# Performance work log

Hardware: AMD Instinct MI355X
Metric: run time of the kernel (lower is better)

## Reference

```python
import jax, jax.numpy as jnp
import numpy as np

N_NODES = 50000
N_EDGES = 1280000
N_GRAPHS = 64
IN_CH = 6
HID = 64
SLOPE = 0.2  # LeakyReLU negative slope


def _lrelu(x):
    return jax.nn.leaky_relu(x, SLOPE)


def _edge_conv(x, src, dst, W1, b1, W2, b2):
    # PyG EdgeConv: message = nn([x_i, x_j - x_i]); x_i = x[dst], x_j = x[src]; max-aggr onto dst
    xi = x[dst]                                   # [E, F]
    m = jnp.concatenate([xi, x[src] - xi], -1)    # [E, 2F]
    h = _lrelu(_lrelu(m @ W1 + b1) @ W2 + b2)     # [E, H]
    agg = jax.ops.segment_max(h, dst, num_segments=N_NODES)
    return jnp.where(jnp.isneginf(agg), 0.0, agg)  # nodes with no in-edges -> 0


def setup_inputs() -> dict:
    key = jax.random.key(0)
    ks = jax.random.split(key, 12)
    glorot = lambda k, fi, fo: jax.random.normal(k, (fi, fo), jnp.float32) * np.sqrt(2.0 / (fi + fo))
    x = jax.random.normal(ks[0], (N_NODES, IN_CH), jnp.float32)
    edge_index = jax.random.randint(ks[1], (2, N_EDGES), 0, N_NODES, jnp.int64 if jax.config.x64_enabled else jnp.int32)
    batch = jnp.sort(jax.random.randint(ks[2], (N_NODES,), 0, N_GRAPHS))
    return {
        "x": x, "edge_index": edge_index, "batch": batch,
        "W1": glorot(ks[3], 2 * IN_CH, HID), "b1": jnp.zeros((HID,), jnp.float32),
        "W2": glorot(ks[4], HID, HID),       "b2": jnp.zeros((HID,), jnp.float32),
        "W3": glorot(ks[5], 2 * HID, HID),   "b3": jnp.zeros((HID,), jnp.float32),
        "W4": glorot(ks[6], HID, HID),       "b4": jnp.zeros((HID,), jnp.float32),
        "Wc1": glorot(ks[7], 2 * HID, HID),  "bc1": jnp.zeros((HID,), jnp.float32),
        "Wc2": glorot(ks[8], HID, 1),        "bc2": jnp.zeros((1,), jnp.float32),
    }


def reference(x, edge_index, batch, W1, b1, W2, b2, W3, b3, W4, b4, Wc1, bc1, Wc2, bc2):
    src, dst = edge_index[0], edge_index[1]
    h = _edge_conv(x, src, dst, W1, b1, W2, b2)   # [N, H]
    h = _edge_conv(h, src, dst, W3, b3, W4, b4)   # [N, H]
    # global mean + max pool per graph
    cnt = jax.ops.segment_sum(jnp.ones((N_NODES,), h.dtype), batch, num_segments=N_GRAPHS)
    mean_p = jax.ops.segment_sum(h, batch, num_segments=N_GRAPHS) / jnp.clip(cnt, 1.0)[:, None]
    max_p = jax.ops.segment_max(h, batch, num_segments=N_GRAPHS)
    max_p = jnp.where(jnp.isneginf(max_p), 0.0, max_p)
    g = jnp.concatenate([mean_p, max_p], -1)      # [G, 2H]
    logits = _lrelu(g @ Wc1 + bc1) @ Wc2 + bc2    # dropout is identity at inference
    return logits.squeeze(-1)                      # [G]
```

## Files before the change

### kernel.cpp

```cpp
#include <hip/hip_runtime.h>
#include <hip/hip_bf16.h>

#define SLOPE 0.2f
#define NPB 64
#define CAP 2048
#define SUBCAP 384
#define MAXBUCK 1024
#define EPB 4096
#define XF1B 512
#define PPARTS 16

typedef _Float16 f16x8  __attribute__((ext_vector_type(8)));
typedef float    f32x4  __attribute__((ext_vector_type(4)));
typedef unsigned u32;
typedef unsigned u32x4  __attribute__((ext_vector_type(4)));

__device__ __forceinline__ float lrelu(float v) { return fmaxf(v, SLOPE * v); }

__device__ __forceinline__ float lane_bcast(float v, int k) {
    return __int_as_float(__builtin_amdgcn_readlane(__float_as_int(v), k));
}

__device__ __forceinline__ f16x8 lrelu8(f16x8 v) {
    f16x8 s = v * (_Float16)SLOPE;
#if __has_builtin(__builtin_elementwise_max)
    return __builtin_elementwise_max(v, s);
#else
    f16x8 r;
#pragma unroll
    for (int i = 0; i < 8; ++i) r[i] = v[i] > s[i] ? v[i] : s[i];
    return r;
#endif
}

__device__ __forceinline__ void split_f16(float v, _Float16& h, _Float16& l) {
    h = (_Float16)v;
    l = (_Float16)(v - (float)h);
}
__device__ __forceinline__ u32 pack_f16(_Float16 a, _Float16 b) {
    return (u32)__builtin_bit_cast(unsigned short, a) |
           ((u32)__builtin_bit_cast(unsigned short, b) << 16);
}

__global__ void __launch_bounds__(256) scatter_xform1_kernel(
    const int* __restrict__ srcI, const int* __restrict__ dstI,
    int* __restrict__ cursor, u32* __restrict__ pairW,
    int E, int nNodes, int nBuck, int nCntB,
    const float* __restrict__ x,
    const float* __restrict__ W1, const float* __restrict__ b1,
    _Float16* __restrict__ Ph, _Float16* __restrict__ Qh)
{
    if (blockIdx.x < nCntB) {
        __shared__ int cnt4[4][MAXBUCK];
        __shared__ int base[MAXBUCK];
// ... 68 lines not shown
        }
        return;
    }
    const int lane = threadIdx.x & 63;
    const int wave = ((blockIdx.x - nCntB) * 256 + threadIdx.x) >> 6;
    const int nw   = (XF1B * 256) >> 6;

    float wd[6], wb[6];
#pragma unroll
    for (int r = 0; r < 6; ++r) {
        wb[r] = W1[(6 + r) * 64 + lane];
        wd[r] = W1[r * 64 + lane] - wb[r];
    }
    const float bb = b1[lane];
    for (int i = wave; i < nNodes; i += nw) {
        const float* xr = x + (size_t)i * 6;
        float p = bb, q = 0.f;
#pragma unroll
        for (int r = 0; r < 6; ++r) {
            float xv = xr[r];
            p = fmaf(xv, wd[r], p);
            q = fmaf(xv, wb[r], q);
        }
        Ph[(size_t)i * 64 + lane] = (_Float16)p;
        Qh[(size_t)i * 64 + lane] = (_Float16)q;
    }
}

__global__ void __launch_bounds__(256) bucket_sort_kernel(
    const u32* __restrict__ pairW, const int* __restrict__ cursor,
    int2* __restrict__ rowInfo, int* __restrict__ sortedSrc, int nNodes)
{
    __shared__ u32 pairLds[CAP];
    __shared__ int nodeCnt[NPB];
    __shared__ int nodeCur[NPB];
    __shared__ int wcS[8];
    __shared__ int wBase[9];
    const int b   = blockIdx.x;
    const int n0  = b * NPB;
    const int n1  = min(n0 + NPB, nNodes);
    const int tid = threadIdx.x;

    if (tid < NPB) nodeCnt[tid] = 0;
    if (tid < 8) wcS[tid] = min(cursor[b * 8 + tid], SUBCAP);
    __syncthreads();
    if (tid == 0) {
        int acc = 0;
#pragma unroll
        for (int jj = 0; jj < 8; ++jj) { wBase[jj] = acc; acc += wcS[jj]; }
        wBase[8] = acc;
    }
    __syncthreads();

#pragma unroll
    for (int jj = 0; jj < 8; ++jj) {
        const int w0 = (b * 8 + jj) * SUBCAP;
        const int wc = wcS[jj];
        const int d0 = wBase[jj];
        const int nv = wc >> 2;
        const u32x4* p4 = (const u32x4*)(pairW + w0);
        for (int i = tid; i < nv; i += 256) {
            const u32x4 v = p4[i];
            pairLds[d0 + i * 4 + 0] = v[0];
            pairLds[d0 + i * 4 + 1] = v[1];
            pairLds[d0 + i * 4 + 2] = v[2];
            pairLds[d0 + i * 4 + 3] = v[3];
        }
        for (int i = (nv << 2) + tid; i < wc; i += 256)
            pairLds[d0 + i] = pairW[w0 + i];
    }
    __syncthreads();

    const int total = wBase[8];
    for (int i = tid; i < total; i += 256)
        atomicAdd(&nodeCnt[pairLds[i] & (NPB - 1)], 1);
    __syncthreads();
    if (tid < 64) {
        const int c = nodeCnt[tid];
        int inc = c;
#pragma unroll
        for (int off = 1; off < 64; off <<= 1) {
            int t = __shfl_up(inc, off);
            if (tid >= off) inc += t;
        }
        const int st = b * CAP + inc - c;
        nodeCur[tid] = st;
        if (tid < n1 - n0) rowInfo[n0 + tid] = make_int2(st, c);
    }
    __syncthreads();
    for (int i = tid; i < total; i += 256) {
        const u32 w = pairLds[i];
        const int pos = atomicAdd(&nodeCur[w & (NPB - 1)], 1);
        sortedSrc[pos] = (int)(w >> 6);
    }
}

__global__ void __launch_bounds__(256) node_xform2_kernel(
    const _Float16* __restrict__ B1h,
    const float* __restrict__ W3, const float* __restrict__ b3,
    _Float16* __restrict__ Ph, _Float16* __restrict__ Qh, int nNodes)
{
    const int lane = threadIdx.x & 63;
    const int wave = (blockIdx.x * blockDim.x + threadIdx.x) >> 6;
    const int nw   = (gridDim.x * blockDim.x) >> 6;

    float wd[64], wb[64];
#pragma unroll
    for (int k = 0; k < 64; ++k) {
        wb[k] = W3[(64 + k) * 64 + lane];
        wd[k] = W3[k * 64 + lane] - wb[k];
    }
    const float bb = b3[lane];

    for (int i = wave; i < nNodes; i += nw) {
        const float a = (float)B1h[(size_t)i * 64 + lane];
        float p0 = bb, p1 = 0.f, p2 = 0.f, p3 = 0.f;
        float q0 = 0.f, q1 = 0.f, q2 = 0.f, q3 = 0.f;
#pragma unroll
        for (int k = 0; k < 64; k += 4) {
            float a0 = lane_bcast(a, k);
            float a1 = lane_bcast(a, k + 1);
            float a2 = lane_bcast(a, k + 2);
            float a3 = lane_bcast(a, k + 3);
            p0 = fmaf(a0, wd[k],     p0);  q0 = fmaf(a0, wb[k],     q0);
            p1 = fmaf(a1, wd[k + 1], p1);  q1 = fmaf(a1, wb[k + 1], q1);
            p2 = fmaf(a2, wd[k + 2], p2);  q2 = fmaf(a2, wb[k + 2], q2);
            p3 = fmaf(a3, wd[k + 3], p3);  q3 = fmaf(a3, wb[k + 3], q3);
        }
        Ph[(size_t)i * 64 + lane] = (_Float16)((p0 + p1) + (p2 + p3));
        Qh[(size_t)i * 64 + lane] = (_Float16)((q0 + q1) + (q2 + q3));
    }
}

__global__ void __launch_bounds__(256) edge_agg_mfma_kernel(
    const _Float16* __restrict__ Ph, const _Float16* __restrict__ Qh,
    const int2* __restrict__ rowInfo, const int* __restrict__ sortedSrc,
    const float* __restrict__ W, const float* __restrict__ b,
    _Float16* __restrict__ outB, int nNodes)
{
    __shared__ u32x4 wlds[16][64];

    const int tid  = threadIdx.x;
    const int lane = tid & 63;
    const int cn   = lane & 15;
    const int q    = lane >> 4;
    const int wv   = tid >> 6;
    const int wave = (blockIdx.x * 256 + tid) >> 6;
    const int nw   = (gridDim.x * 256) >> 6;

#pragma unroll
    for (int i = 0; i < 4; ++i) {
        const int f    = wv + i * 4;
        const int isLo = f >> 3;
        const int g    = f & 7;
        const int nt   = g >> 1;
        const int ks   = g & 1;
        u32x4 d;
#pragma unroll
        for (int p = 0; p < 4; ++p) {
            float w0 = W[(ks * 32 + q * 8 + 2 * p)     * 64 + nt * 16 + cn];
            float w1 = W[(ks * 32 + q * 8 + 2 * p + 1) * 64 + nt * 16 + cn];
            _Float16 h0, l0, h1, l1;
            split_f16(w0, h0, l0);
            split_f16(w1, h1, l1);
            d[p] = isLo ? pack_f16(l0, l1) : pack_f16(h0, h1);
        }
        wlds[f][lane] = d;
    }
    float bc[4];
#pragma unroll
    for (int nt = 0; nt < 4; ++nt) bc[nt] = b[nt * 16 + cn];
    __syncthreads();

    const u32 nClamp = (u32)(nNodes - 1);
    const int nPairs = (nNodes + 1) >> 1;

    for (int t = wave; t < nPairs; t += nw) {
        const int n1 = 2 * t;
        const int n2 = 2 * t + 1;
        const bool has2 = (n2 < nNodes);

        const int2 ri1 = rowInfo[n1];
        const int2 ri2 = has2 ? rowInfo[n2] : make_int2(ri1.x, 0);
        const int rs1  = __builtin_amdgcn_readfirstlane(ri1.x);
        const int deg1 = __builtin_amdgcn_readfirstlane(ri1.y);
        const int rs2  = __builtin_amdgcn_readfirstlane(ri2.x);
        const int deg2 = __builtin_amdgcn_readfirstlane(ri2.y);
        const int d1c = max(deg1, 1) - 1;
        const int d2c = max(deg2, 1) - 1;

        const f16x8* P1 = (const f16x8*)(Ph + (size_t)n1 * 64);
        const f16x8* P2 = (const f16x8*)(Ph + (size_t)(has2 ? n2 : n1) * 64);
        const f16x8 p1A = P1[q], p1B = P1[4 + q];
        const f16x8 p2A = P2[q], p2B = P2[4 + q];

        float m10 = -INFINITY, m11 = -INFINITY, m12 = -INFINITY, m13 = -INFINITY;
        float m20 = -INFINITY, m21 = -INFINITY, m22 = -INFINITY, m23 = -INFINITY;

        const int gmax = max(deg1, deg2);
        for (int g0 = 0; g0 < gmax; g0 += 32) {
            u32 sA1 = (u32)sortedSrc[rs1 + min(g0 + cn,      d1c)];
            u32 sB1 = (u32)sortedSrc[rs1 + min(g0 + 16 + cn, d1c)];
            u32 sA2 = (u32)sortedSrc[rs2 + min(g0 + cn,      d2c)];
            u32 sB2 = (u32)sortedSrc[rs2 + min(g0 + 16 + cn, d2c)];
            sA1 = min(sA1, nClamp); sB1 = min(sB1, nClamp);
            sA2 = min(sA2, nClamp); sB2 = min(sB2, nClamp);
            const f16x8* QA1 = (const f16x8*)(Qh + (size_t)sA1 * 64);
            const f16x8* QB1 = (const f16x8*)(Qh + (size_t)sB1 * 64);
            const f16x8* QA2 = (const f16x8*)(Qh + (size_t)sA2 * 64);
            const f16x8* QB2 = (const f16x8*)(Qh + (size_t)sB2 * 64);
            const f16x8 qA1a = QA1[q], qA1b = QA1[4 + q];
            const f16x8 qB1a = QB1[q], qB1b = QB1[4 + q];
            const f16x8 qA2a = QA2[q], qA2b = QA2[4 + q];
            const f16x8 qB2a = QB2[q], qB2b = QB2[4 + q];

            if (g0 < deg1) {
                const f16x8 A00 = lrelu8(p1A + qA1a);
                const f16x8 A01 = lrelu8(p1B + qA1b);
                const f16x8 A10 = lrelu8(p1A + qB1a);
                const f16x8 A11 = lrelu8(p1B + qB1b);
#pragma unroll
                for (int nt = 0; nt < 4; ++nt) {
                    const f16x8 wh0 = __builtin_bit_cast(f16x8, wlds[nt * 2][lane]);
                    const f16x8 wh1 = __builtin_bit_cast(f16x8, wlds[nt * 2 + 1][lane]);
                    const f16x8 wl0 = __builtin_bit_cast(f16x8, wlds[8 + nt * 2][lane]);
                    const f16x8 wl1 = __builtin_bit_cast(f16x8, wlds[8 + nt * 2 + 1][lane]);
                    f32x4 a; a[0] = a[1] = a[2] = a[3] = bc[nt];
                    a = __builtin_amdgcn_mfma_f32_16x16x32_f16(A00, wl0, a, 0, 0, 0);
                    a = __builtin_amdgcn_mfma_f32_16x16x32_f16(A00, wh0, a, 0, 0, 0);
                    a = __builtin_amdgcn_mfma_f32_16x16x32_f16(A01, wl1, a, 0, 0, 0);
                    a = __builtin_amdgcn_mfma_f32_16x16x32_f16(A01, wh1, a, 0, 0, 0);
                    f32x4 c; c[0] = c[1] = c[2] = c[3] = bc[nt];
                    c = __builtin_amdgcn_mfma_f32_16x16x32_f16(A10, wl0, c, 0, 0, 0);
                    c = __builtin_amdgcn_mfma_f32_16x16x32_f16(A10, wh0, c, 0, 0, 0);
                    c = __builtin_amdgcn_mfma_f32_16x16x32_f16(A11, wl1, c, 0, 0, 0);
                    c = __builtin_amdgcn_mfma_f32_16x16x32_f16(A11, wh1, c, 0, 0, 0);
                    float m = (nt == 0) ? m10 : (nt == 1) ? m11 : (nt == 2) ? m12 : m13;
                    m = fmaxf(m, fmaxf(fmaxf(a[0], a[1]), fmaxf(a[2], a[3])));
                    m = fmaxf(m, fmaxf(fmaxf(c[0], c[1]), fmaxf(c[2], c[3])));
                    if (nt == 0) m10 = m; else if (nt == 1) m11 = m;
                    else if (nt == 2) m12 = m; else m13 = m;
                }
            }
            if (g0 < deg2) {
                const f16x8 A00 = lrelu8(p2A + qA2a);
                const f16x8 A01 = lrelu8(p2B + qA2b);
                const f16x8 A10 = lrelu8(p2A + qB2a);
                const f16x8 A11 = lrelu8(p2B + qB2b);
#pragma unroll
                for (int nt = 0; nt < 4; ++nt) {
                    const f16x8 wh0 = __builtin_bit_cast(f16x8, wlds[nt * 2][lane]);
                    const f16x8 wh1 = __builtin_bit_cast(f16x8, wlds[nt * 2 + 1][lane]);
                    const f16x8 wl0 = __builtin_bit_cast(f16x8, wlds[8 + nt * 2][lane]);
                    const f16x8 wl1 = __builtin_bit_cast(f16x8, wlds[8 + nt * 2 + 1][lane]);
                    f32x4 a; a[0] = a[1] = a[2] = a[3] = bc[nt];
                    a = __builtin_amdgcn_mfma_f32_16x16x32_f16(A00, wl0, a, 0, 0, 0);
                    a = __builtin_amdgcn_mfma_f32_16x16x32_f16(A00, wh0, a, 0, 0, 0);
                    a = __builtin_amdgcn_mfma_f32_16x16x32_f16(A01, wl1, a, 0, 0, 0);
                    a = __builtin_amdgcn_mfma_f32_16x16x32_f16(A01, wh1, a, 0, 0, 0);
                    f32x4 c; c[0] = c[1] = c[2] = c[3] = bc[nt];
                    c = __builtin_amdgcn_mfma_f32_16x16x32_f16(A10, wl0, c, 0, 0, 0);
                    c = __builtin_amdgcn_mfma_f32_16x16x32_f16(A10, wh0, c, 0, 0, 0);
                    c = __builtin_amdgcn_mfma_f32_16x16x32_f16(A11, wl1, c, 0, 0, 0);
                    c = __builtin_amdgcn_mfma_f32_16x16x32_f16(A11, wh1, c, 0, 0, 0);
                    float m = (nt == 0) ? m20 : (nt == 1) ? m21 : (nt == 2) ? m22 : m23;
                    m = fmaxf(m, fmaxf(fmaxf(a[0], a[1]), fmaxf(a[2], a[3])));
                    m = fmaxf(m, fmaxf(fmaxf(c[0], c[1]), fmaxf(c[2], c[3])));
                    if (nt == 0) m20 = m; else if (nt == 1) m21 = m;
                    else if (nt == 2) m22 = m; else m23 = m;
                }
            }
        }

        m10 = fmaxf(m10, __shfl_xor(m10, 16)); m10 = fmaxf(m10, __shfl_xor(m10, 32));
        m11 = fmaxf(m11, __shfl_xor(m11, 16)); m11 = fmaxf(m11, __shfl_xor(m11, 32));
        m12 = fmaxf(m12, __shfl_xor(m12, 16)); m12 = fmaxf(m12, __shfl_xor(m12, 32));
        m13 = fmaxf(m13, __shfl_xor(m13, 16)); m13 = fmaxf(m13, __shfl_xor(m13, 32));
        float sel1 = (q < 2) ? ((q == 0) ? m10 : m11) : ((q == 2) ? m12 : m13);
        outB[(size_t)n1 * 64 + q * 16 + cn] =
            (_Float16)((deg1 > 0) ? lrelu(sel1) : 0.0f);

        if (has2) {
            m20 = fmaxf(m20, __shfl_xor(m20, 16)); m20 = fmaxf(m20, __shfl_xor(m20, 32));
            m21 = fmaxf(m21, __shfl_xor(m21, 16)); m21 = fmaxf(m21, __shfl_xor(m21, 32));
            m22 = fmaxf(m22, __shfl_xor(m22, 16)); m22 = fmaxf(m22, __shfl_xor(m22, 32));
            m23 = fmaxf(m23, __shfl_xor(m23, 16)); m23 = fmaxf(m23, __shfl_xor(m23, 32));
            float sel2 = (q < 2) ? ((q == 0) ? m20 : m21) : ((q == 2) ? m22 : m23);
            outB[(size_t)n2 * 64 + q * 16 + cn] =
                (_Float16)((deg2 > 0) ? lrelu(sel2) : 0.0f);
        }
    }
}

__device__ __forceinline__ int lower_bound_i(const int* __restrict__ a, int n, int key)
{
    int lo = 0, hi = n;
    while (lo < hi) {
        int mid = (lo + hi) >> 1;
        if (a[mid] < key) lo = mid + 1; else hi = mid;
    }
    return lo;
}

__global__ void __launch_bounds__(256) pool_kernel(
    const _Float16* __restrict__ Bh, const int* __restrict__ batch,
    float* __restrict__ gpart, int nNodes)
{
    const int gid  = blockIdx.x / PPARTS;
    const int part = blockIdx.x % PPARTS;
    const int c    = threadIdx.x & 63;
    const int wid  = threadIdx.x >> 6;

    const int s = lower_bound_i(batch, nNodes, gid);
    const int e = lower_bound_i(batch, nNodes, gid + 1);
    const int len = e - s;
    const int ps = s + (len * part) / PPARTS;
    const int pe = s + (len * (part + 1)) / PPARTS;

    float sum = 0.f, mx = -INFINITY;
    for (int n = ps + wid; n < pe; n += 4) {
        float v = (float)Bh[(size_t)n * 64 + c];
        sum += v;
        mx = fmaxf(mx, v);
// ... 68 lines not shown
    const float* bc2 = (const float*)d_in[14];
    float* out = (float*)d_out;

    const int nNodes  = in_sizes[0] / 6;
    const int E       = in_sizes[1] / 2;
    const int nGraphs = out_size;
    const int* srcI = ei;
    const int* dstI = ei + E;
    const int nBuck = (nNodes + NPB - 1) / NPB;
    const int nCntB = (E + EPB - 1) / EPB;

    char* wsp = (char*)d_ws;
    size_t off = 0;
    int*  cursor    = (int*)(wsp + off);   off = align_up(off + (size_t)MAXBUCK * 8 * 4, 256);
    int2* rowInfo   = (int2*)(wsp + off);  off = align_up(off + (size_t)nNodes * 8, 256);
    int*  sortedSrc = (int*)(wsp + off);   off = align_up(off + (size_t)nBuck * CAP * 4, 256);
    u32*  pairW     = (u32*)(wsp + off);   off = align_up(off + (size_t)nBuck * 8 * SUBCAP * 4, 256);
    const size_t nFeat = (size_t)nNodes * 64;
    _Float16* Ph   = (_Float16*)(wsp + off);  off = align_up(off + nFeat * 2, 256);
    _Float16* Qh   = (_Float16*)(wsp + off);  off = align_up(off + nFeat * 2, 256);
    _Float16* B1h  = (_Float16*)(wsp + off);  off = align_up(off + nFeat * 2, 256);
    _Float16* B2h  = (_Float16*)(wsp + off);  off = align_up(off + nFeat * 2, 256);
    float*    gpart= (float*)(wsp + off);     off = align_up(off + (size_t)nGraphs * PPARTS * 132 * 4, 256);
    (void)ws_size;

    (void)hipMemsetAsync(cursor, 0, (size_t)nBuck * 8 * 4, stream);
    scatter_xform1_kernel<<<nCntB + XF1B, 256, 0, stream>>>(
        srcI, dstI, cursor, pairW, E, nNodes, nBuck, nCntB, x, W1, b1, Ph, Qh);
    bucket_sort_kernel<<<nBuck, 256, 0, stream>>>(pairW, cursor, rowInfo,
                                                  sortedSrc, nNodes);

    edge_agg_mfma_kernel<<<2048, 256, 0, stream>>>(Ph, Qh, rowInfo, sortedSrc,
                                                   W2, b2, B1h, nNodes);
    node_xform2_kernel<<<2048, 256, 0, stream>>>(B1h, W3, b3, Ph, Qh, nNodes);
    edge_agg_mfma_kernel<<<2048, 256, 0, stream>>>(Ph, Qh, rowInfo, sortedSrc,
                                                   W4, b4, B2h, nNodes);

    pool_kernel<<<nGraphs * PPARTS, 256, 0, stream>>>(B2h, batch, gpart, nNodes);
    cls_kernel<<<nGraphs, 64, 0, stream>>>(gpart, Wc1, bc1, Wc2, bc2, out);
}
```

Baseline: 267.7 us.

## Software-pipeline edge aggregation with one node per wave and prefetched gathers

The edge aggregation kernel now gives each wave one destination node per iteration instead of a pair, and software-pipelines across iterations. It prefetches the next node's row info, source indices, P row and first batch of Q gathers while computing the current node. This aims to hide gather latency without the wasted lanes and divergence that come from processing two nodes of unequal degree together. It also adds an occupancy hint to the launch bounds, which may limit registers and cause spills given the larger set of live prefetch buffers.

```diff
diff --git a/kernel.cpp b/kernel.cpp
--- a/kernel.cpp
+++ b/kernel.cpp
@@ -254,7 +254,7 @@
     }
 }
 
-__global__ void __launch_bounds__(256) edge_agg_mfma_kernel(
+__global__ void __launch_bounds__(256, 4) edge_agg_mfma_kernel(
     const _Float16* __restrict__ Ph, const _Float16* __restrict__ Qh,
     const int2* __restrict__ rowInfo, const int* __restrict__ sortedSrc,
     const float* __restrict__ W, const float* __restrict__ b,
@@ -294,122 +294,121 @@
     for (int nt = 0; nt < 4; ++nt) bc[nt] = b[nt * 16 + cn];
     __syncthreads();
 
+    if (wave >= nNodes) return;
+
     const u32 nClamp = (u32)(nNodes - 1);
-    const int nPairs = (nNodes + 1) >> 1;
-
-    for (int t = wave; t < nPairs; t += nw) {
-        const int n1 = 2 * t;
-        const int n2 = 2 * t + 1;
-        const bool has2 = (n2 < nNodes);
-
-        const int2 ri1 = rowInfo[n1];
-        const int2 ri2 = has2 ? rowInfo[n2] : make_int2(ri1.x, 0);
-        const int rs1  = __builtin_amdgcn_readfirstlane(ri1.x);
-        const int deg1 = __builtin_amdgcn_readfirstlane(ri1.y);
-        const int rs2  = __builtin_amdgcn_readfirstlane(ri2.x);
-        const int deg2 = __builtin_amdgcn_readfirstlane(ri2.y);
-        const int d1c = max(deg1, 1) - 1;
-        const int d2c = max(deg2, 1) - 1;
-
-        const f16x8* P1 = (const f16x8*)(Ph + (size_t)n1 * 64);
-        const f16x8* P2 = (const f16x8*)(Ph + (size_t)(has2 ? n2 : n1) * 64);
-        const f16x8 p1A = P1[q], p1B = P1[4 + q];
-        const f16x8 p2A = P2[q], p2B = P2[4 + q];
-
-        float m10 = -INFINITY, m11 = -INFINITY, m12 = -INFINITY, m13 = -INFINITY;
-        float m20 = -INFINITY, m21 = -INFINITY, m22 = -INFINITY, m23 = -INFINITY;
-
-        const int gmax = max(deg1, deg2);
-        for (int g0 = 0; g0 < gmax; g0 += 32) {
-            u32 sA1 = (u32)sortedSrc[rs1 + min(g0 + cn,      d1c)];
-            u32 sB1 = (u32)sortedSrc[rs1 + min(g0 + 16 + cn, d1c)];
-            u32 sA2 = (u32)sortedSrc[rs2 + min(g0 + cn,      d2c)];
-            u32 sB2 = (u32)sortedSrc[rs2 + min(g0 + 16 + cn, d2c)];
-            sA1 = min(sA1, nClamp); sB1 = min(sB1, nClamp);
-            sA2 = min(sA2, nClamp); sB2 = min(sB2, nClamp);
-            const f16x8* QA1 = (const f16x8*)(Qh + (size_t)sA1 * 64);
-            const f16x8* QB1 = (const f16x8*)(Qh + (size_t)sB1 * 64);
-            const f16x8* QA2 = (const f16x8*)(Qh + (size_t)sA2 * 64);
-            const f16x8* QB2 = (const f16x8*)(Qh + (size_t)sB2 * 64);
-            const f16x8 qA1a = QA1[q], qA1b = QA1[4 + q];
-            const f16x8 qB1a = QB1[q], qB1b = QB1[4 + q];
-            const f16x8 qA2a = QA2[q], qA2b = QA2[4 + q];
-            const f16x8 qB2a = QB2[q], qB2b = QB2[4 + q];
-
-            if (g0 < deg1) {
-                const f16x8 A00 = lrelu8(p1A + qA1a);
-                const f16x8 A01 = lrelu8(p1B + qA1b);
-                const f16x8 A10 = lrelu8(p1A + qB1a);
-                const f16x8 A11 = lrelu8(p1B + qB1b);
-#pragma unroll
-                for (int nt = 0; nt < 4; ++nt) {
-                    const f16x8 wh0 = __builtin_bit_cast(f16x8, wlds[nt * 2][lane]);
-                    const f16x8 wh1 = __builtin_bit_cast(f16x8, wlds[nt * 2 + 1][lane]);
-                    const f16x8 wl0 = __builtin_bit_cast(f16x8, wlds[8 + nt * 2][lane]);
-                    const f16x8 wl1 = __builtin_bit_cast(f16x8, wlds[8 + nt * 2 + 1][lane]);
-                    f32x4 a; a[0] = a[1] = a[2] = a[3] = bc[nt];
-                    a = __builtin_amdgcn_mfma_f32_16x16x32_f16(A00, wl0, a, 0, 0, 0);
-                    a = __builtin_amdgcn_mfma_f32_16x16x32_f16(A00, wh0, a, 0, 0, 0);
-                    a = __builtin_amdgcn_mfma_f32_16x16x32_f16(A01, wl1, a, 0, 0, 0);
-                    a = __builtin_amdgcn_mfma_f32_16x16x32_f16(A01, wh1, a, 0, 0, 0);
-                    f32x4 c; c[0] = c[1] = c[2] = c[3] = bc[nt];
-                    c = __builtin_amdgcn_mfma_f32_16x16x32_f16(A10, wl0, c, 0, 0, 0);
-                    c = __builtin_amdgcn_mfma_f32_16x16x32_f16(A10, wh0, c, 0, 0, 0);
-                    c = __builtin_amdgcn_mfma_f32_16x16x32_f16(A11, wl1, c, 0, 0, 0);
-                    c = __builtin_amdgcn_mfma_f32_16x16x32_f16(A11, wh1, c, 0, 0, 0);
-                    float m = (nt == 0) ? m10 : (nt == 1) ? m11 : (nt == 2) ? m12 : m13;
-                    m = fmaxf(m, fmaxf(fmaxf(a[0], a[1]), fmaxf(a[2], a[3])));
-                    m = fmaxf(m, fmaxf(fmaxf(c[0], c[1]), fmaxf(c[2], c[3])));
-                    if (nt == 0) m10 = m; else if (nt == 1) m11 = m;
-                    else if (nt == 2) m12 = m; else m13 = m;
-                }
+    const int nLast  = nNodes - 1;
+
+    auto loadIdx = [&](int rs, int dc, int g0, u32& sA, u32& sB) {
+        sA = (u32)sortedSrc[rs + min(g0 + cn, dc)];
+        sB = (u32)sortedSrc[rs + min(g0 + 16 + cn, dc)];
+    };
+    auto loadQ = [&](u32 sA, u32 sB, f16x8& qAa, f16x8& qAb,
+                     f16x8& qBa, f16x8& qBb) {
+        const f16x8* QA = (const f16x8*)(Qh + (size_t)min(sA, nClamp) * 64);
+        const f16x8* QB = (const f16x8*)(Qh + (size_t)min(sB, nClamp) * 64);
+        qAa = QA[q]; qAb = QA[4 + q];
+        qBa = QB[q]; qBb = QB[4 + q];
+    };
+    auto loadP = [&](int t, f16x8& pA, f16x8& pB) {
+        const f16x8* P = (const f16x8*)(Ph + (size_t)t * 64);
+        pA = P[q]; pB = P[4 + q];
+    };
+    auto compute32 = [&](f16x8 pA, f16x8 pB,
+                         f16x8 qAa, f16x8 qAb, f16x8 qBa, f16x8 qBb,
+                         float& m0, float& m1, float& m2, float& m3) {
+        const f16x8 A00 = lrelu8(pA + qAa);
+        const f16x8 A01 = lrelu8(pB + qAb);
+        const f16x8 A10 = lrelu8(pA + qBa);
+        const f16x8 A11 = lrelu8(pB + qBb);
+#pragma unroll
+        for (int nt = 0; nt < 4; ++nt) {
+            const f16x8 wh0 = __builtin_bit_cast(f16x8, wlds[nt * 2][lane]);
+            const f16x8 wh1 = __builtin_bit_cast(f16x8, wlds[nt * 2 + 1][lane]);
+            const f16x8 wl0 = __builtin_bit_cast(f16x8, wlds[8 + nt * 2][lane]);
+            const f16x8 wl1 = __builtin_bit_cast(f16x8, wlds[8 + nt * 2 + 1][lane]);
+            f32x4 a; a[0] = a[1] = a[2] = a[3] = bc[nt];
+            a = __builtin_amdgcn_mfma_f32_16x16x32_f16(A00, wl0, a, 0, 0, 0);
+            a = __builtin_amdgcn_mfma_f32_16x16x32_f16(A00, wh0, a, 0, 0, 0);
+            a = __builtin_amdgcn_mfma_f32_16x16x32_f16(A01, wl1, a, 0, 0, 0);
+            a = __builtin_amdgcn_mfma_f32_16x16x32_f16(A01, wh1, a, 0, 0, 0);
+            f32x4 c; c[0] = c[1] = c[2] = c[3] = bc[nt];
+            c = __builtin_amdgcn_mfma_f32_16x16x32_f16(A10, wl0, c, 0, 0, 0);
+            c = __builtin_amdgcn_mfma_f32_16x16x32_f16(A10, wh0, c, 0, 0, 0);
+            c = __builtin_amdgcn_mfma_f32_16x16x32_f16(A11, wl1, c, 0, 0, 0);
+            c = __builtin_amdgcn_mfma_f32_16x16x32_f16(A11, wh1, c, 0, 0, 0);
+            float m = (nt == 0) ? m0 : (nt == 1) ? m1 : (nt == 2) ? m2 : m3;
+            m = fmaxf(fmaxf(fmaxf(a[0], a[1]), a[2]), fmaxf(a[3], m));
+            m = fmaxf(fmaxf(fmaxf(c[0], c[1]), c[2]), fmaxf(c[3], m));
+            if (nt == 0) m0 = m; else if (nt == 1) m1 = m;
+            else if (nt == 2) m2 = m; else m3 = m;
+        }
+    };
+
+    f16x8 q0Aa, q0Ab, q0Ba, q0Bb, p0A, p0B;  u32 s0A, s0B;
+    f16x8 q1Aa, q1Ab, q1Ba, q1Bb, p1A, p1B;  u32 s1A, s1B;
+    int2 riN;
+    int rs0, dg0, rs1, dg1;
+
+    {
+        const int2 riA = rowInfo[wave];
+        const int2 riB = rowInfo[min(wave + nw, nLast)];
+        rs0 = __builtin_amdgcn_readfirstlane(riA.x);
+        dg0 = __builtin_amdgcn_readfirstlane(riA.y);
+        rs1 = __builtin_amdgcn_readfirstlane(riB.x);
+        dg1 = __builtin_amdgcn_readfirstlane(riB.y);
+        loadIdx(rs0, max(dg0, 1) - 1, 0, s0A, s0B);
+        loadP(wave, p0A, p0B);
+        loadQ(s0A, s0B, q0Aa, q0Ab, q0Ba, q0Bb);
+        loadIdx(rs1, max(dg1, 1) - 1, 0, s1A, s1B);
+        loadP(min(wave + nw, nLast), p1A, p1B);
+        riN = rowInfo[min(wave + 2 * nw, nLast)];
+    }
+
+    auto iter = [&](int tc, int rsC, int dgC, int& rs2, int& dg2,
+                    f16x8& qCAa, f16x8& qCAb, f16x8& qCBa, f16x8& qCBb,
+                    f16x8& pCA, f16x8& pCB, u32& sCA, u32& sCB,
+                    f16x8& qNAa, f16x8& qNAb, f16x8& qNBa, f16x8& qNBb,
+                    u32 sNA, u32 sNB) {
+        loadQ(sNA, sNB, qNAa, qNAb, qNBa, qNBb);
+        rs2 = __builtin_amdgcn_readfirstlane(riN.x);
+        dg2 = __builtin_amdgcn_readfirstlane(riN.y);
+        loadIdx(rs2, max(dg2, 1) - 1, 0, sCA, sCB);
+        riN = rowInfo[min(tc + 3 * nw, nLast)];
+        float m0 = -INFINITY, m1 = -INFINITY, m2 = -INFINITY, m3 = -INFINITY;
+        if (dgC > 0) {
+            compute32(pCA, pCB, qCAa, qCAb, qCBa, qCBb, m0, m1, m2, m3);
+            const int dcC = dgC - 1;
+            for (int g0 = 32; g0 < dgC; g0 += 32) {
+                u32 eA, eB;
+                loadIdx(rsC, dcC, g0, eA, eB);
+                f16x8 eAa, eAb, eBa, eBb;
+                loadQ(eA, eB, eAa, eAb, eBa, eBb);
+                compute32(pCA, pCB, eAa, eAb, eBa, eBb, m0, m1, m2, m3);
             }
-            if (g0 < deg2) {
-                const f16x8 A00 = lrelu8(p2A + qA2a);
-                const f16x8 A01 = lrelu8(p2B + qA2b);
-                const f16x8 A10 = lrelu8(p2A + qB2a);
-                const f16x8 A11 = lrelu8(p2B + qB2b);
-#pragma unroll
-                for (int nt = 0; nt < 4; ++nt) {
-                    const f16x8 wh0 = __builtin_bit_cast(f16x8, wlds[nt * 2][lane]);
-                    const f16x8 wh1 = __builtin_bit_cast(f16x8, wlds[nt * 2 + 1][lane]);
-                    const f16x8 wl0 = __builtin_bit_cast(f16x8, wlds[8 + nt * 2][lane]);
-                    const f16x8 wl1 = __builtin_bit_cast(f16x8, wlds[8 + nt * 2 + 1][lane]);
-                    f32x4 a; a[0] = a[1] = a[2] = a[3] = bc[nt];
-                    a = __builtin_amdgcn_mfma_f32_16x16x32_f16(A00, wl0, a, 0, 0, 0);
-                    a = __builtin_amdgcn_mfma_f32_16x16x32_f16(A00, wh0, a, 0, 0, 0);
-                    a = __builtin_amdgcn_mfma_f32_16x16x32_f16(A01, wl1, a, 0, 0, 0);
-                    a = __builtin_amdgcn_mfma_f32_16x16x32_f16(A01, wh1, a, 0, 0, 0);
-                    f32x4 c; c[0] = c[1] = c[2] = c[3] = bc[nt];
-                    c = __builtin_amdgcn_mfma_f32_16x16x32_f16(A10, wl0, c, 0, 0, 0);
-                    c = __builtin_amdgcn_mfma_f32_16x16x32_f16(A10, wh0, c, 0, 0, 0);
-                    c = __builtin_amdgcn_mfma_f32_16x16x32_f16(A11, wl1, c, 0, 0, 0);
-                    c = __builtin_amdgcn_mfma_f32_16x16x32_f16(A11, wh1, c, 0, 0, 0);
-                    float m = (nt == 0) ? m20 : (nt == 1) ? m21 : (nt == 2) ? m22 : m23;
-                    m = fmaxf(m, fmaxf(fmaxf(a[0], a[1]), fmaxf(a[2], a[3])));
-                    m = fmaxf(m, fmaxf(fmaxf(c[0], c[1]), fmaxf(c[2], c[3])));
-                    if (nt == 0) m20 = m; else if (nt == 1) m21 = m;
-                    else if (nt == 2) m22 = m; else m23 = m;
-                }
-            }
-        }
-
-        m10 = fmaxf(m10, __shfl_xor(m10, 16)); m10 = fmaxf(m10, __shfl_xor(m10, 32));
-        m11 = fmaxf(m11, __shfl_xor(m11, 16)); m11 = fmaxf(m11, __shfl_xor(m11, 32));
-        m12 = fmaxf(m12, __shfl_xor(m12, 16)); m12 = fmaxf(m12, __shfl_xor(m12, 32));
-        m13 = fmaxf(m13, __shfl_xor(m13, 16)); m13 = fmaxf(m13, __shfl_xor(m13, 32));
-        float sel1 = (q < 2) ? ((q == 0) ? m10 : m11) : ((q == 2) ? m12 : m13);
-        outB[(size_t)n1 * 64 + q * 16 + cn] =
-            (_Float16)((deg1 > 0) ? lrelu(sel1) : 0.0f);
-
-        if (has2) {
-            m20 = fmaxf(m20, __shfl_xor(m20, 16)); m20 = fmaxf(m20, __shfl_xor(m20, 32));
-            m21 = fmaxf(m21, __shfl_xor(m21, 16)); m21 = fmaxf(m21, __shfl_xor(m21, 32));
-            m22 = fmaxf(m22, __shfl_xor(m22, 16)); m22 = fmaxf(m22, __shfl_xor(m22, 32));
-            m23 = fmaxf(m23, __shfl_xor(m23, 16)); m23 = fmaxf(m23, __shfl_xor(m23, 32));
-            float sel2 = (q < 2) ? ((q == 0) ? m20 : m21) : ((q == 2) ? m22 : m23);
-            outB[(size_t)n2 * 64 + q * 16 + cn] =
-                (_Float16)((deg2 > 0) ? lrelu(sel2) : 0.0f);
+        }
+        loadP(min(tc + 2 * nw, nLast), pCA, pCB);
+        m0 = fmaxf(m0, __shfl_xor(m0, 16)); m0 = fmaxf(m0, __shfl_xor(m0, 32));
+        m1 = fmaxf(m1, __shfl_xor(m1, 16)); m1 = fmaxf(m1, __shfl_xor(m1, 32));
+        m2 = fmaxf(m2, __shfl_xor(m2, 16)); m2 = fmaxf(m2, __shfl_xor(m2, 32));
+        m3 = fmaxf(m3, __shfl_xor(m3, 16)); m3 = fmaxf(m3, __shfl_xor(m3, 32));
+        const float sel = (q < 2) ? ((q == 0) ? m0 : m1)
+                                  : ((q == 2) ? m2 : m3);
+        outB[(size_t)tc * 64 + q * 16 + cn] =
+            (_Float16)((dgC > 0) ? lrelu(sel) : 0.0f);
+    };
+
+    for (int t = wave; t < nNodes; t += 2 * nw) {
+        int rs2, dg2;
+        iter(t, rs0, dg0, rs2, dg2,
+             q0Aa, q0Ab, q0Ba, q0Bb, p0A, p0B, s0A, s0B,
+             q1Aa, q1Ab, q1Ba, q1Bb, s1A, s1B);
+        rs0 = rs2; dg0 = dg2;
+        if (t + nw < nNodes) {
+            iter(t + nw, rs1, dg1, rs2, dg2,
+                 q1Aa, q1Ab, q1Ba, q1Bb, p1A, p1B, s1A, s1B,
+                 q0Aa, q0Ab, q0Ba, q0Bb, s0A, s0B);
+            rs1 = rs2; dg1 = dg2;
         }
     }
 }
```

Measured after the change: 468.6 us. 1.75x slower.

## Software-pipeline row info and source index loads across node-pair iterations

Applied to the files above, without the earlier changes.

Restructures the edge aggregation loop so that the rowInfo for the pair two iterations ahead and the first 32 sortedSrc indices for the next pair are loaded ahead of time and carried in registers. The first 32-edge chunk is then processed straight from the prefetched indices, and later chunks fall back to the original per-chunk loads. This targets the dependent load chain (rowInfo, then sortedSrc, then Qh) that stalls each wave at the start of every pair, at the cost of more live registers and extra prefetch loads. The MFMA body is factored into a macro, with a small reordering of the max reduction.

```diff
diff --git a/kernel.cpp b/kernel.cpp
--- a/kernel.cpp
+++ b/kernel.cpp
@@ -254,6 +254,37 @@
     }
 }
 
+
+#define COMPUTE32(PA, PB, QA0, QA1, QB0, QB1, M0, M1, M2, M3)                  \
+  {                                                                            \
+    const f16x8 A00_ = lrelu8((PA) + (QA0));                                   \
+    const f16x8 A01_ = lrelu8((PB) + (QA1));                                   \
+    const f16x8 A10_ = lrelu8((PA) + (QB0));                                   \
+    const f16x8 A11_ = lrelu8((PB) + (QB1));                                   \
+    _Pragma("unroll")                                                          \
+    for (int nt_ = 0; nt_ < 4; ++nt_) {                                        \
+      const f16x8 wh0_ = __builtin_bit_cast(f16x8, wlds[nt_ * 2][lane]);       \
+      const f16x8 wh1_ = __builtin_bit_cast(f16x8, wlds[nt_ * 2 + 1][lane]);   \
+      const f16x8 wl0_ = __builtin_bit_cast(f16x8, wlds[8 + nt_ * 2][lane]);   \
+      const f16x8 wl1_ = __builtin_bit_cast(f16x8, wlds[8 + nt_ * 2 + 1][lane]); \
+      f32x4 a_; a_[0] = a_[1] = a_[2] = a_[3] = bc[nt_];                       \
+      a_ = __builtin_amdgcn_mfma_f32_16x16x32_f16(A00_, wl0_, a_, 0, 0, 0);    \
+      a_ = __builtin_amdgcn_mfma_f32_16x16x32_f16(A00_, wh0_, a_, 0, 0, 0);    \
+      a_ = __builtin_amdgcn_mfma_f32_16x16x32_f16(A01_, wl1_, a_, 0, 0, 0);    \
+      a_ = __builtin_amdgcn_mfma_f32_16x16x32_f16(A01_, wh1_, a_, 0, 0, 0);    \
+      f32x4 c_; c_[0] = c_[1] = c_[2] = c_[3] = bc[nt_];                       \
+      c_ = __builtin_amdgcn_mfma_f32_16x16x32_f16(A10_, wl0_, c_, 0, 0, 0);    \
+      c_ = __builtin_amdgcn_mfma_f32_16x16x32_f16(A10_, wh0_, c_, 0, 0, 0);    \
+      c_ = __builtin_amdgcn_mfma_f32_16x16x32_f16(A11_, wl1_, c_, 0, 0, 0);    \
+      c_ = __builtin_amdgcn_mfma_f32_16x16x32_f16(A11_, wh1_, c_, 0, 0, 0);    \
+      float m_ = (nt_ == 0) ? (M0) : (nt_ == 1) ? (M1) : (nt_ == 2) ? (M2) : (M3); \
+      m_ = fmaxf(fmaxf(fmaxf(a_[0], a_[1]), a_[2]), fmaxf(a_[3], m_));         \
+      m_ = fmaxf(fmaxf(fmaxf(c_[0], c_[1]), c_[2]), fmaxf(c_[3], m_));         \
+      if (nt_ == 0) (M0) = m_; else if (nt_ == 1) (M1) = m_;                   \
+      else if (nt_ == 2) (M2) = m_; else (M3) = m_;                            \
+    }                                                                          \
+  }
+
 __global__ void __launch_bounds__(256) edge_agg_mfma_kernel(
     const _Float16* __restrict__ Ph, const _Float16* __restrict__ Qh,
     const int2* __restrict__ rowInfo, const int* __restrict__ sortedSrc,
@@ -294,104 +325,93 @@
     for (int nt = 0; nt < 4; ++nt) bc[nt] = b[nt * 16 + cn];
     __syncthreads();
 
+    const int nPairs = (nNodes + 1) >> 1;
+    if (wave >= nPairs) return;
     const u32 nClamp = (u32)(nNodes - 1);
-    const int nPairs = (nNodes + 1) >> 1;
+    const int nLastN = nNodes - 1;
+    const int pLast  = nPairs - 1;
+
+    int rs1, dg1, rs2, dg2;
+    u32 sA1, sB1, sA2, sB2;
+    int2 riNa, riNb;
+
+    {
+        const int n1 = 2 * wave;
+        const int2 r1 = rowInfo[n1];
+        const int2 r2 = rowInfo[min(n1 + 1, nLastN)];
+        rs1 = __builtin_amdgcn_readfirstlane(r1.x);
+        dg1 = __builtin_amdgcn_readfirstlane(r1.y);
+        rs2 = __builtin_amdgcn_readfirstlane(r2.x);
+        dg2 = __builtin_amdgcn_readfirstlane(r2.y);
+        const int d1c = max(dg1, 1) - 1;
+        const int d2c = max(dg2, 1) - 1;
+        sA1 = (u32)sortedSrc[rs1 + min(cn, d1c)];
+        sB1 = (u32)sortedSrc[rs1 + min(16 + cn, d1c)];
+        sA2 = (u32)sortedSrc[rs2 + min(cn, d2c)];
+        sB2 = (u32)sortedSrc[rs2 + min(16 + cn, d2c)];
+        const int tn = min(wave + nw, pLast);
+        riNa = rowInfo[2 * tn];
+        riNb = rowInfo[min(2 * tn + 1, nLastN)];
+    }
 
     for (int t = wave; t < nPairs; t += nw) {
         const int n1 = 2 * t;
-        const int n2 = 2 * t + 1;
+        const int n2 = n1 + 1;
         const bool has2 = (n2 < nNodes);
-
-        const int2 ri1 = rowInfo[n1];
-        const int2 ri2 = has2 ? rowInfo[n2] : make_int2(ri1.x, 0);
-        const int rs1  = __builtin_amdgcn_readfirstlane(ri1.x);
-        const int deg1 = __builtin_amdgcn_readfirstlane(ri1.y);
-        const int rs2  = __builtin_amdgcn_readfirstlane(ri2.x);
-        const int deg2 = __builtin_amdgcn_readfirstlane(ri2.y);
-        const int d1c = max(deg1, 1) - 1;
-        const int d2c = max(deg2, 1) - 1;
-
+        const int dg2e = has2 ? dg2 : 0;
+        const int d1c = max(dg1, 1) - 1;
+        const int d2c = max(dg2, 1) - 1;
+
+        const f16x8* QA1 = (const f16x8*)(Qh + (size_t)min(sA1, nClamp) * 64);
+        const f16x8* QB1 = (const f16x8*)(Qh + (size_t)min(sB1, nClamp) * 64);
+        const f16x8* QA2 = (const f16x8*)(Qh + (size_t)min(sA2, nClamp) * 64);
+        const f16x8* QB2 = (const f16x8*)(Qh + (size_t)min(sB2, nClamp) * 64);
+        const f16x8 qA1a = QA1[q], qA1b = QA1[4 + q];
+        const f16x8 qB1a = QB1[q], qB1b = QB1[4 + q];
+        const f16x8 qA2a = QA2[q], qA2b = QA2[4 + q];
+        const f16x8 qB2a = QB2[q], qB2b = QB2[4 + q];
         const f16x8* P1 = (const f16x8*)(Ph + (size_t)n1 * 64);
-        const f16x8* P2 = (const f16x8*)(Ph + (size_t)(has2 ? n2 : n1) * 64);
+        const f16x8* P2 = (const f16x8*)(Ph + (size_t)min(n2, nLastN) * 64);
         const f16x8 p1A = P1[q], p1B = P1[4 + q];
         const f16x8 p2A = P2[q], p2B = P2[4 + q];
 
+        const int rsN1 = __builtin_amdgcn_readfirstlane(riNa.x);
+        const int dgN1 = __builtin_amdgcn_readfirstlane(riNa.y);
+        const int rsN2 = __builtin_amdgcn_readfirstlane(riNb.x);
+        const int dgN2 = __builtin_amdgcn_readfirstlane(riNb.y);
+        const int dN1c = max(dgN1, 1) - 1;
+        const int dN2c = max(dgN2, 1) - 1;
+        const u32 sNA1 = (u32)sortedSrc[rsN1 + min(cn, dN1c)];
+        const u32 sNB1 = (u32)sortedSrc[rsN1 + min(16 + cn, dN1c)];
+        const u32 sNA2 = (u32)sortedSrc[rsN2 + min(cn, dN2c)];
+        const u32 sNB2 = (u32)sortedSrc[rsN2 + min(16 + cn, dN2c)];
+        {
+            const int t2 = min(t + 2 * nw, pLast);
+            riNa = rowInfo[2 * t2];
+            riNb = rowInfo[min(2 * t2 + 1, nLastN)];
+        }
+
         float m10 = -INFINITY, m11 = -INFINITY, m12 = -INFINITY, m13 = -INFINITY;
         float m20 = -INFINITY, m21 = -INFINITY, m22 = -INFINITY, m23 = -INFINITY;
-
-        const int gmax = max(deg1, deg2);
-        for (int g0 = 0; g0 < gmax; g0 += 32) {
-            u32 sA1 = (u32)sortedSrc[rs1 + min(g0 + cn,      d1c)];
-            u32 sB1 = (u32)sortedSrc[rs1 + min(g0 + 16 + cn, d1c)];
-            u32 sA2 = (u32)sortedSrc[rs2 + min(g0 + cn,      d2c)];
-            u32 sB2 = (u32)sortedSrc[rs2 + min(g0 + 16 + cn, d2c)];
-            sA1 = min(sA1, nClamp); sB1 = min(sB1, nClamp);
-            sA2 = min(sA2, nClamp); sB2 = min(sB2, nClamp);
-            const f16x8* QA1 = (const f16x8*)(Qh + (size_t)sA1 * 64);
-            const f16x8* QB1 = (const f16x8*)(Qh + (size_t)sB1 * 64);
-            const f16x8* QA2 = (const f16x8*)(Qh + (size_t)sA2 * 64);
-            const f16x8* QB2 = (const f16x8*)(Qh + (size_t)sB2 * 64);
-            const f16x8 qA1a = QA1[q], qA1b = QA1[4 + q];
-            const f16x8 qB1a = QB1[q], qB1b = QB1[4 + q];
-            const f16x8 qA2a = QA2[q], qA2b = QA2[4 + q];
-            const f16x8 qB2a = QB2[q], qB2b = QB2[4 + q];
-
-            if (g0 < deg1) {
-                const f16x8 A00 = lrelu8(p1A + qA1a);
-                const f16x8 A01 = lrelu8(p1B + qA1b);
-                const f16x8 A10 = lrelu8(p1A + qB1a);
-                const f16x8 A11 = lrelu8(p1B + qB1b);
-#pragma unroll
-                for (int nt = 0; nt < 4; ++nt) {
-                    const f16x8 wh0 = __builtin_bit_cast(f16x8, wlds[nt * 2][lane]);
-                    const f16x8 wh1 = __builtin_bit_cast(f16x8, wlds[nt * 2 + 1][lane]);
-                    const f16x8 wl0 = __builtin_bit_cast(f16x8, wlds[8 + nt * 2][lane]);
-                    const f16x8 wl1 = __builtin_bit_cast(f16x8, wlds[8 + nt * 2 + 1][lane]);
-                    f32x4 a; a[0] = a[1] = a[2] = a[3] = bc[nt];
-                    a = __builtin_amdgcn_mfma_f32_16x16x32_f16(A00, wl0, a, 0, 0, 0);
-                    a = __builtin_amdgcn_mfma_f32_16x16x32_f16(A00, wh0, a, 0, 0, 0);
-                    a = __builtin_amdgcn_mfma_f32_16x16x32_f16(A01, wl1, a, 0, 0, 0);
-                    a = __builtin_amdgcn_mfma_f32_16x16x32_f16(A01, wh1, a, 0, 0, 0);
-                    f32x4 c; c[0] = c[1] = c[2] = c[3] = bc[nt];
-                    c = __builtin_amdgcn_mfma_f32_16x16x32_f16(A10, wl0, c, 0, 0, 0);
-                    c = __builtin_amdgcn_mfma_f32_16x16x32_f16(A10, wh0, c, 0, 0, 0);
-                    c = __builtin_amdgcn_mfma_f32_16x16x32_f16(A11, wl1, c, 0, 0, 0);
-                    c = __builtin_amdgcn_mfma_f32_16x16x32_f16(A11, wh1, c, 0, 0, 0);
-                    float m = (nt == 0) ? m10 : (nt == 1) ? m11 : (nt == 2) ? m12 : m13;
-                    m = fmaxf(m, fmaxf(fmaxf(a[0], a[1]), fmaxf(a[2], a[3])));
-                    m = fmaxf(m, fmaxf(fmaxf(c[0], c[1]), fmaxf(c[2], c[3])));
-                    if (nt == 0) m10 = m; else if (nt == 1) m11 = m;
-                    else if (nt == 2) m12 = m; else m13 = m;
-                }
-            }
-            if (g0 < deg2) {
-                const f16x8 A00 = lrelu8(p2A + qA2a);
-                const f16x8 A01 = lrelu8(p2B + qA2b);
-                const f16x8 A10 = lrelu8(p2A + qB2a);
-                const f16x8 A11 = lrelu8(p2B + qB2b);
-#pragma unroll
-                for (int nt = 0; nt < 4; ++nt) {
-                    const f16x8 wh0 = __builtin_bit_cast(f16x8, wlds[nt * 2][lane]);
-                    const f16x8 wh1 = __builtin_bit_cast(f16x8, wlds[nt * 2 + 1][lane]);
-                    const f16x8 wl0 = __builtin_bit_cast(f16x8, wlds[8 + nt * 2][lane]);
-                    const f16x8 wl1 = __builtin_bit_cast(f16x8, wlds[8 + nt * 2 + 1][lane]);
-                    f32x4 a; a[0] = a[1] = a[2] = a[3] = bc[nt];
-                    a = __builtin_amdgcn_mfma_f32_16x16x32_f16(A00, wl0, a, 0, 0, 0);
-                    a = __builtin_amdgcn_mfma_f32_16x16x32_f16(A00, wh0, a, 0, 0, 0);
-                    a = __builtin_amdgcn_mfma_f32_16x16x32_f16(A01, wl1, a, 0, 0, 0);
-                    a = __builtin_amdgcn_mfma_f32_16x16x32_f16(A01, wh1, a, 0, 0, 0);
-                    f32x4 c; c[0] = c[1] = c[2] = c[3] = bc[nt];
-                    c = __builtin_amdgcn_mfma_f32_16x16x32_f16(A10, wl0, c, 0, 0, 0);
-                    c = __builtin_amdgcn_mfma_f32_16x16x32_f16(A10, wh0, c, 0, 0, 0);
-                    c = __builtin_amdgcn_mfma_f32_16x16x32_f16(A11, wl1, c, 0, 0, 0);
-                    c = __builtin_amdgcn_mfma_f32_16x16x32_f16(A11, wh1, c, 0, 0, 0);
-                    float m = (nt == 0) ? m20 : (nt == 1) ? m21 : (nt == 2) ? m22 : m23;
-                    m = fmaxf(m, fmaxf(fmaxf(a[0], a[1]), fmaxf(a[2], a[3])));
-                    m = fmaxf(m, fmaxf(fmaxf(c[0], c[1]), fmaxf(c[2], c[3])));
-                    if (nt == 0) m20 = m; else if (nt == 1) m21 = m;
-                    else if (nt == 2) m22 = m; else m23 = m;
-                }
-            }
+        if (dg1 > 0)  COMPUTE32(p1A, p1B, qA1a, qA1b, qB1a, qB1b, m10, m11, m12, m13);
+        if (dg2e > 0) COMPUTE32(p2A, p2B, qA2a, qA2b, qB2a, qB2b, m20, m21, m22, m23);
+
+        const int gmax = max(dg1, dg2e);
+        for (int g0 = 32; g0 < gmax; g0 += 32) {
+            u32 eA1 = (u32)sortedSrc[rs1 + min(g0 + cn,      d1c)];
+            u32 eB1 = (u32)sortedSrc[rs1 + min(g0 + 16 + cn, d1c)];
+            u32 eA2 = (u32)sortedSrc[rs2 + min(g0 + cn,      d2c)];
+            u32 eB2 = (u32)sortedSrc[rs2 + min(g0 + 16 + cn, d2c)];
+            const f16x8* EA1 = (const f16x8*)(Qh + (size_t)min(eA1, nClamp) * 64);
+            const f16x8* EB1 = (const f16x8*)(Qh + (size_t)min(eB1, nClamp) * 64);
+            const f16x8* EA2 = (const f16x8*)(Qh + (size_t)min(eA2, nClamp) * 64);
+            const f16x8* EB2 = (const f16x8*)(Qh + (size_t)min(eB2, nClamp) * 64);
+            const f16x8 gA1a = EA1[q], gA1b = EA1[4 + q];
+            const f16x8 gB1a = EB1[q], gB1b = EB1[4 + q];
+            const f16x8 gA2a = EA2[q], gA2b = EA2[4 + q];
+            const f16x8 gB2a = EB2[q], gB2b = EB2[4 + q];
+            if (g0 < dg1)  COMPUTE32(p1A, p1B, gA1a, gA1b, gB1a, gB1b, m10, m11, m12, m13);
+            if (g0 < dg2e) COMPUTE32(p2A, p2B, gA2a, gA2b, gB2a, gB2b, m20, m21, m22, m23);
         }
 
         m10 = fmaxf(m10, __shfl_xor(m10, 16)); m10 = fmaxf(m10, __shfl_xor(m10, 32));
@@ -400,7 +420,7 @@
         m13 = fmaxf(m13, __shfl_xor(m13, 16)); m13 = fmaxf(m13, __shfl_xor(m13, 32));
         float sel1 = (q < 2) ? ((q == 0) ? m10 : m11) : ((q == 2) ? m12 : m13);
         outB[(size_t)n1 * 64 + q * 16 + cn] =
-            (_Float16)((deg1 > 0) ? lrelu(sel1) : 0.0f);
+            (_Float16)((dg1 > 0) ? lrelu(sel1) : 0.0f);
 
         if (has2) {
             m20 = fmaxf(m20, __shfl_xor(m20, 16)); m20 = fmaxf(m20, __shfl_xor(m20, 32));
@@ -409,8 +429,11 @@
             m23 = fmaxf(m23, __shfl_xor(m23, 16)); m23 = fmaxf(m23, __shfl_xor(m23, 32));
             float sel2 = (q < 2) ? ((q == 0) ? m20 : m21) : ((q == 2) ? m22 : m23);
             outB[(size_t)n2 * 64 + q * 16 + cn] =
-                (_Float16)((deg2 > 0) ? lrelu(sel2) : 0.0f);
-        }
+                (_Float16)((dg2e > 0) ? lrelu(sel2) : 0.0f);
+        }
+
+        rs1 = rsN1; dg1 = dgN1; rs2 = rsN2; dg2 = dgN2;
+        sA1 = sNA1; sB1 = sNB1; sA2 = sNA2; sB2 = sNB2;
     }
 }
 
```

Result: no change. 272.3 us (+1.7%).

## Use MFMA for second node transform and per-wave counters in bucket sort

Applied to the files above, without the earlier changes.

The per-node 64x128 transform before the second EdgeConv moves from scalar FMAs with lane broadcasts onto f16 MFMA tiles. Weights are split into hi/lo f16 parts staged in LDS so the f16 matrix units keep close to fp32 accuracy, and the grid is sized to one 16-node group per wave. Separately, the bucket sort gives each wave its own LDS histogram and cursor array to reduce atomic contention. In exchange, each block rebuilds the split weights, and the sorted order within a node now depends on wave id.

```diff
diff --git a/kernel.cpp b/kernel.cpp
--- a/kernel.cpp
+++ b/kernel.cpp
@@ -16,10 +16,6 @@
 typedef unsigned u32x4  __attribute__((ext_vector_type(4)));
 
 __device__ __forceinline__ float lrelu(float v) { return fmaxf(v, SLOPE * v); }
-
-__device__ __forceinline__ float lane_bcast(float v, int k) {
-    return __int_as_float(__builtin_amdgcn_readlane(__float_as_int(v), k));
-}
 
 __device__ __forceinline__ f16x8 lrelu8(f16x8 v) {
     f16x8 s = v * (_Float16)SLOPE;
@@ -154,16 +150,20 @@
     int2* __restrict__ rowInfo, int* __restrict__ sortedSrc, int nNodes)
 {
     __shared__ u32 pairLds[CAP];
-    __shared__ int nodeCnt[NPB];
-    __shared__ int nodeCur[NPB];
+    __shared__ int nodeCnt4[4][NPB];
+    __shared__ int nodeCur4[4][NPB];
     __shared__ int wcS[8];
     __shared__ int wBase[9];
     const int b   = blockIdx.x;
     const int n0  = b * NPB;
     const int n1  = min(n0 + NPB, nNodes);
     const int tid = threadIdx.x;
-
-    if (tid < NPB) nodeCnt[tid] = 0;
+    const int wv  = tid >> 6;
+
+    if (tid < NPB) {
+        nodeCnt4[0][tid] = 0; nodeCnt4[1][tid] = 0;
+        nodeCnt4[2][tid] = 0; nodeCnt4[3][tid] = 0;
+    }
     if (tid < 8) wcS[tid] = min(cursor[b * 8 + tid], SUBCAP);
     __syncthreads();
     if (tid == 0) {
@@ -195,10 +195,12 @@
 
     const int total = wBase[8];
     for (int i = tid; i < total; i += 256)
-        atomicAdd(&nodeCnt[pairLds[i] & (NPB - 1)], 1);
+        atomicAdd(&nodeCnt4[wv][pairLds[i] & (NPB - 1)], 1);
     __syncthreads();
     if (tid < 64) {
-        const int c = nodeCnt[tid];
+        const int c0 = nodeCnt4[0][tid], c1 = nodeCnt4[1][tid];
+        const int c2 = nodeCnt4[2][tid], c3 = nodeCnt4[3][tid];
+        const int c = (c0 + c1) + (c2 + c3);
         int inc = c;
 #pragma unroll
         for (int off = 1; off < 64; off <<= 1) {
@@ -206,51 +208,112 @@
             if (tid >= off) inc += t;
         }
         const int st = b * CAP + inc - c;
-        nodeCur[tid] = st;
+        nodeCur4[0][tid] = st;
+        nodeCur4[1][tid] = st + c0;
+        nodeCur4[2][tid] = st + c0 + c1;
+        nodeCur4[3][tid] = st + c0 + c1 + c2;
         if (tid < n1 - n0) rowInfo[n0 + tid] = make_int2(st, c);
     }
     __syncthreads();
     for (int i = tid; i < total; i += 256) {
         const u32 w = pairLds[i];
-        const int pos = atomicAdd(&nodeCur[w & (NPB - 1)], 1);
+        const int pos = atomicAdd(&nodeCur4[wv][w & (NPB - 1)], 1);
         sortedSrc[pos] = (int)(w >> 6);
     }
 }
 
-__global__ void __launch_bounds__(256) node_xform2_kernel(
+__global__ void __launch_bounds__(256) node_xform2_mfma_kernel(
     const _Float16* __restrict__ B1h,
     const float* __restrict__ W3, const float* __restrict__ b3,
     _Float16* __restrict__ Ph, _Float16* __restrict__ Qh, int nNodes)
 {
-    const int lane = threadIdx.x & 63;
-    const int wave = (blockIdx.x * blockDim.x + threadIdx.x) >> 6;
-    const int nw   = (gridDim.x * blockDim.x) >> 6;
-
-    float wd[64], wb[64];
-#pragma unroll
-    for (int k = 0; k < 64; ++k) {
-        wb[k] = W3[(64 + k) * 64 + lane];
-        wd[k] = W3[k * 64 + lane] - wb[k];
-    }
-    const float bb = b3[lane];
-
-    for (int i = wave; i < nNodes; i += nw) {
-        const float a = (float)B1h[(size_t)i * 64 + lane];
-        float p0 = bb, p1 = 0.f, p2 = 0.f, p3 = 0.f;
-        float q0 = 0.f, q1 = 0.f, q2 = 0.f, q3 = 0.f;
-#pragma unroll
-        for (int k = 0; k < 64; k += 4) {
-            float a0 = lane_bcast(a, k);
-            float a1 = lane_bcast(a, k + 1);
-            float a2 = lane_bcast(a, k + 2);
-            float a3 = lane_bcast(a, k + 3);
-            p0 = fmaf(a0, wd[k],     p0);  q0 = fmaf(a0, wb[k],     q0);
-            p1 = fmaf(a1, wd[k + 1], p1);  q1 = fmaf(a1, wb[k + 1], q1);
-            p2 = fmaf(a2, wd[k + 2], p2);  q2 = fmaf(a2, wb[k + 2], q2);
-            p3 = fmaf(a3, wd[k + 3], p3);  q3 = fmaf(a3, wb[k + 3], q3);
-        }
-        Ph[(size_t)i * 64 + lane] = (_Float16)((p0 + p1) + (p2 + p3));
-        Qh[(size_t)i * 64 + lane] = (_Float16)((q0 + q1) + (q2 + q3));
+    __shared__ u32x4 wlds[32][64];
+
+    const int tid  = threadIdx.x;
+    const int lane = tid & 63;
+    const int cn   = lane & 15;
+    const int q    = lane >> 4;
+    const int wv   = tid >> 6;
+    const int wave = (blockIdx.x * 256 + tid) >> 6;
+    const int nw   = (gridDim.x * 256) >> 6;
+
+#pragma unroll
+    for (int i = 0; i < 8; ++i) {
+        const int f    = wv + i * 4;
+        const int isLo = f >> 4;
+        const int g    = f & 15;
+        const int nt   = g >> 1;
+        const int ks   = g & 1;
+        const int col  = (nt & 3) * 16 + cn;
+        u32x4 d;
+#pragma unroll
+        for (int p = 0; p < 4; ++p) {
+            const int k0 = ks * 32 + q * 8 + 2 * p;
+            float w0, w1;
+            if (nt < 4) {
+                w0 = W3[k0 * 64 + col]       - W3[(64 + k0) * 64 + col];
+                w1 = W3[(k0 + 1) * 64 + col] - W3[(64 + k0 + 1) * 64 + col];
+            } else {
+                w0 = W3[(64 + k0) * 64 + col];
+                w1 = W3[(64 + k0 + 1) * 64 + col];
+            }
+            _Float16 h0, l0, h1, l1;
+            split_f16(w0, h0, l0);
+            split_f16(w1, h1, l1);
+            d[p] = isLo ? pack_f16(l0, l1) : pack_f16(h0, h1);
+        }
+        wlds[f][lane] = d;
+    }
+    float bcv[4];
+#pragma unroll
+    for (int nt = 0; nt < 4; ++nt) bcv[nt] = b3[nt * 16 + cn];
+    __syncthreads();
+
+    const int nGrp = (nNodes + 15) >> 4;
+    for (int t = wave; t < nGrp; t += nw) {
+        const int n0 = t << 4;
+        const int rA = min(n0 + cn, nNodes - 1);
+        const f16x8* Arow = (const f16x8*)(B1h + (size_t)rA * 64);
+        const f16x8 A0 = Arow[q];
+        const f16x8 A1 = Arow[4 + q];
+
+        f32x4 acc0, acc1, acc2, acc3, acc4, acc5, acc6, acc7;
+#define NT_TILE(ACC, NT, INI)                                                  \
+        {                                                                      \
+            const f16x8 wh0 = __builtin_bit_cast(f16x8, wlds[(NT) * 2][lane]); \
+            const f16x8 wh1 = __builtin_bit_cast(f16x8, wlds[(NT) * 2 + 1][lane]); \
+            const f16x8 wl0 = __builtin_bit_cast(f16x8, wlds[16 + (NT) * 2][lane]); \
+            const f16x8 wl1 = __builtin_bit_cast(f16x8, wlds[16 + (NT) * 2 + 1][lane]); \
+            f32x4 a_; a_[0] = a_[1] = a_[2] = a_[3] = (INI);                   \
+            a_ = __builtin_amdgcn_mfma_f32_16x16x32_f16(A0, wl0, a_, 0, 0, 0); \
+            a_ = __builtin_amdgcn_mfma_f32_16x16x32_f16(A0, wh0, a_, 0, 0, 0); \
+            a_ = __builtin_amdgcn_mfma_f32_16x16x32_f16(A1, wl1, a_, 0, 0, 0); \
+            a_ = __builtin_amdgcn_mfma_f32_16x16x32_f16(A1, wh1, a_, 0, 0, 0); \
+            ACC = a_;                                                          \
+        }
+        NT_TILE(acc0, 0, bcv[0]); NT_TILE(acc1, 1, bcv[1]);
+        NT_TILE(acc2, 2, bcv[2]); NT_TILE(acc3, 3, bcv[3]);
+        NT_TILE(acc4, 4, 0.0f);   NT_TILE(acc5, 5, 0.0f);
+        NT_TILE(acc6, 6, 0.0f);   NT_TILE(acc7, 7, 0.0f);
+#undef NT_TILE
+
+        const int rowLim = nNodes - n0;
+#pragma unroll
+        for (int j = 0; j < 4; ++j) {
+            const int r = 4 * q + j;
+            if (r < rowLim) {
+                _Float16* Pr = Ph + (size_t)(n0 + r) * 64;
+                _Float16* Qr = Qh + (size_t)(n0 + r) * 64;
+                Pr[cn]      = (_Float16)acc0[j];
+                Pr[16 + cn] = (_Float16)acc1[j];
+                Pr[32 + cn] = (_Float16)acc2[j];
+                Pr[48 + cn] = (_Float16)acc3[j];
+                Qr[cn]      = (_Float16)acc4[j];
+                Qr[16 + cn] = (_Float16)acc5[j];
+                Qr[32 + cn] = (_Float16)acc6[j];
+                Qr[48 + cn] = (_Float16)acc7[j];
+            }
+        }
     }
 }
 
@@ -545,7 +608,10 @@
 
     edge_agg_mfma_kernel<<<2048, 256, 0, stream>>>(Ph, Qh, rowInfo, sortedSrc,
                                                    W2, b2, B1h, nNodes);
-    node_xform2_kernel<<<2048, 256, 0, stream>>>(B1h, W3, b3, Ph, Qh, nNodes);
+    const int nGrp   = (nNodes + 15) >> 4;
+    const int xf2Blk = (nGrp + 3) >> 2;
+    node_xform2_mfma_kernel<<<xf2Blk, 256, 0, stream>>>(B1h, W3, b3, Ph, Qh,
+                                                        nNodes);
     edge_agg_mfma_kernel<<<2048, 256, 0, stream>>>(Ph, Qh, rowInfo, sortedSrc,
                                                    W4, b4, B2h, nNodes);
 
```

Result: faster. 261.4 us (-2.3%).
